# Optimization experiments

Hardware: AMD Instinct MI355X
Metric: run time of the kernel (lower is better)

The kernel has to match this reference:

```python
import jax, jax.numpy as jnp
import numpy as np

KERNEL_SIZE = 32
KERNEL_STRIDE = 16
HEAD_NUM_K = 4
HEAD_DIM = 128
BATCH = 4
SEQ_LEN = 16384


def _calc_chunks_with_stride(cu_seqlens_np, chunk_size, stride):
    """Mirror of calc_chunks_with_stride using numpy (index computation on host).

    Returns flat gather indices (num_chunks*chunk_size,) and compressed
    cumulative sequence lengths (batch+1,).
    """
    cu = np.asarray(cu_seqlens_np, dtype=np.int64)
    batch_sizes = cu[1:] - cu[:-1]
    max_seq_len = int(batch_sizes.max())
    max_chunks = max((max_seq_len - chunk_size) // stride + 1, 0)
    offsets = np.arange(0, max_chunks * stride, stride, dtype=np.int64)  # (C,)
    seq_starts = cu[:-1]
    chunk_start = seq_starts[:, None] + offsets[None, :]            # (B, C)
    chunk_end = chunk_start + chunk_size
    valid = chunk_end <= (seq_starts[:, None] + batch_sizes[:, None])  # (B, C)
    valid_starts = chunk_start[valid]                               # (N,)
    inner = np.arange(chunk_size, dtype=np.int64)[None, :]          # (1, K)
    flat_idx = (valid_starts[:, None] + inner).reshape(-1)          # (N*K,)
    n_per_batch = valid.sum(axis=1)
    cu_comp = np.zeros(len(cu), dtype=np.int32)
    cu_comp[1:] = np.cumsum(n_per_batch)
    return flat_idx, cu_comp


def setup_inputs() -> dict:
    key = jax.random.key(0)
    k = jax.random.normal(key, (BATCH * SEQ_LEN, HEAD_NUM_K, HEAD_DIM), dtype=jnp.float32)
    cu_seqlens = jnp.arange(BATCH + 1, dtype=jnp.int32) * SEQ_LEN
    return {"k": k, "cu_seqlens": cu_seqlens}


def reference(k, cu_seqlens):
    # Index computation is data-dependent on concrete cu_seqlens (host-side).
    flat_idx, cu_comp = _calc_chunks_with_stride(np.asarray(cu_seqlens), KERNEL_SIZE, KERNEL_STRIDE)
    idx = jnp.asarray(flat_idx)
    # Gather overlapping chunks: (N*K, H, D) -> (N, K, H, D) -> mean over K.
    gathered = k[idx]
    gathered = gathered.reshape(-1, KERNEL_SIZE, HEAD_NUM_K, HEAD_DIM)
    compressed_k = gathered.mean(axis=1)
    return compressed_k, jnp.asarray(cu_comp)
```

## Files before the change

kernel.cpp:

```cpp
#include <hip/hip_runtime.h>

#define KSIZE   32
#define KSTRIDE 16
#define HK      4
#define HD      128
#define ROW     (HK * HD)
#define ROW4    (ROW / 4)
#define BATCH   4
#define SEQLEN  16384
#define CHUNKS_PER_BATCH ((SEQLEN - KSIZE) / KSTRIDE + 1)
#define TOTAL_CHUNKS     (BATCH * CHUNKS_PER_BATCH)
#define HW_PER_BATCH     (SEQLEN / KSTRIDE)
#define TOTAL_HW         (BATCH * HW_PER_BATCH)
#define WS_FLOATS        ((size_t)TOTAL_HW * ROW)


__global__ __launch_bounds__(128)
void hw_sums(const float* __restrict__ k,
             const int* __restrict__ cu_seqlens,
             float* __restrict__ H) {
    const int j  = blockIdx.x;
    const int b  = j >> 10;
    const int hw = j & (HW_PER_BATCH - 1);
    const float4* __restrict__ src = (const float4*)
        (k + ((long)cu_seqlens[b] + (long)hw * KSTRIDE) * ROW);
    const int t = threadIdx.x;

    float4 a0 = make_float4(0.f, 0.f, 0.f, 0.f);
    float4 a1 = make_float4(0.f, 0.f, 0.f, 0.f);
    #pragma unroll
    for (int r = 0; r < KSTRIDE; r += 2) {
        float4 u = src[(long)r * ROW4 + t];
        float4 v = src[(long)(r + 1) * ROW4 + t];
        a0.x += u.x; a0.y += u.y; a0.z += u.z; a0.w += u.w;
        a1.x += v.x; a1.y += v.y; a1.z += v.z; a1.w += v.w;
    }
    float4 s = make_float4(a0.x + a1.x, a0.y + a1.y, a0.z + a1.z, a0.w + a1.w);
    ((float4*)(H + (long)j * ROW))[t] = s;
}

__global__ __launch_bounds__(256)
void hw_combine(const float* __restrict__ H,
                const int* __restrict__ cu_seqlens,
                float* __restrict__ out,
                float* __restrict__ tail) {
    const int idx = blockIdx.x * 256 + threadIdx.x;
    if (idx < TOTAL_CHUNKS * ROW4) {
        const int chunk = idx >> 7;
        const int col   = idx & (ROW4 - 1);
        const int b     = chunk / CHUNKS_PER_BATCH;
        const int c     = chunk - b * CHUNKS_PER_BATCH;

        const long h = ((long)(b * HW_PER_BATCH + c)) * ROW4 + col;
        float4 u = ((const float4*)H)[h];
        float4 v = ((const float4*)H)[h + ROW4];
        const float s = 1.0f / (float)KSIZE;
        float4 r = make_float4((u.x + v.x) * s, (u.y + v.y) * s,
                               (u.z + v.z) * s, (u.w + v.w) * s);
        ((float4*)out)[(long)chunk * ROW4 + col] = r;
    }

    if (idx == 0) {
        int run = 0;
        tail[0] = 0.0f;
        #pragma unroll
        for (int i = 0; i < BATCH; ++i) {
            const int len = cu_seqlens[i + 1] - cu_seqlens[i];
            const int n = (len >= KSIZE) ? (len - KSIZE) / KSTRIDE + 1 : 0;
            run += n;
            tail[i + 1] = (float)run;
        }
    }
}

#define SPAN 8
#define FB_BLOCKS_PER_BATCH ((CHUNKS_PER_BATCH + SPAN - 1) / SPAN)
#define FB_TOTAL_BLOCKS     (BATCH * FB_BLOCKS_PER_BATCH)

__device__ __forceinline__ float4 sum16(const float4* __restrict__ src,
                                        int row0, int t) {
    float4 a0 = make_float4(0.f, 0.f, 0.f, 0.f);
    float4 a1 = make_float4(0.f, 0.f, 0.f, 0.f);
    #pragma unroll
    for (int i = 0; i < 8; ++i) {
        float4 u = src[(long)(row0 + 2 * i)     * ROW4 + t];
        float4 v = src[(long)(row0 + 2 * i + 1) * ROW4 + t];
        a0.x += u.x; a0.y += u.y; a0.z += u.z; a0.w += u.w;
        a1.x += v.x; a1.y += v.y; a1.z += v.z; a1.w += v.w;
    }
    a0.x += a1.x; a0.y += a1.y; a0.z += a1.z; a0.w += a1.w;
    return a0;
}

__global__ __launch_bounds__(128)
void compress_k_fallback(const float* __restrict__ k,
                         const int* __restrict__ cu_seqlens,
                         float* __restrict__ out,
                         float* __restrict__ tail) {
    const int blk = blockIdx.x;
    const int b   = blk / FB_BLOCKS_PER_BATCH;
    const int cb  = blk - b * FB_BLOCKS_PER_BATCH;
    const int c0  = cb * SPAN;
    const int gc  = (CHUNKS_PER_BATCH - c0 < SPAN) ? (CHUNKS_PER_BATCH - c0)
                                                   : SPAN;
    const float4* __restrict__ src = (const float4*)
        (k + ((long)cu_seqlens[b] + (long)c0 * KSTRIDE) * ROW);
    const int t = threadIdx.x;
    const float s = 1.0f / (float)KSIZE;
    float* outp = out + (long)(b * CHUNKS_PER_BATCH + c0) * ROW;

    float4 prev = sum16(src, 0, t);
    for (int g = 0; g < gc; ++g) {
        float4 cur = sum16(src, (g + 1) * KSTRIDE, t);
        float4 r = make_float4((prev.x + cur.x) * s, (prev.y + cur.y) * s,
                               (prev.z + cur.z) * s, (prev.w + cur.w) * s);
        ((float4*)(outp + (long)g * ROW))[t] = r;
        prev = cur;
    }
    if (blk == 0 && t == 0) {
        int run = 0;
        tail[0] = 0.0f;
        #pragma unroll
        for (int i = 0; i < BATCH; ++i) {
            const int len = cu_seqlens[i + 1] - cu_seqlens[i];
            const int n = (len >= KSIZE) ? (len - KSIZE) / KSTRIDE + 1 : 0;
            run += n;
            tail[i + 1] = (float)run;
        }
    }
}

extern "C" void kernel_launch(void* const* d_in, const int* in_sizes, int n_in,
                              void* d_out, int out_size, void* d_ws, size_t ws_size,
                              hipStream_t stream) {
    const float* k          = (const float*)d_in[0];
    const int*   cu_seqlens = (const int*)d_in[1];
    float*       out        = (float*)d_out;
    float*       tail       = out + (long)TOTAL_CHUNKS * ROW;

    if (ws_size >= WS_FLOATS * sizeof(float) && d_ws != nullptr) {
        float* H = (float*)d_ws;
        hw_sums<<<TOTAL_HW, 128, 0, stream>>>(k, cu_seqlens, H);
        const int p2_threads = TOTAL_CHUNKS * ROW4;
        const int p2_blocks  = (p2_threads + 255) / 256;
        hw_combine<<<p2_blocks, 256, 0, stream>>>(H, cu_seqlens, out, tail);
    } else {
        compress_k_fallback<<<FB_TOTAL_BLOCKS, 128, 0, stream>>>(
            k, cu_seqlens, out, tail);
    }
}
```

Before: 195.6 us.

## Compute even chunks inside the partial-sum pass and combine only odd chunks after

The first pass now handles two consecutive stride-16 windows per block, writes both partial sums to the workspace, and directly emits the even-indexed compressed chunk. The second pass only combines partial sums for odd-indexed chunks, halving its reads and writes. This trades fewer, larger first-pass blocks for less intermediate memory traffic in the second kernel.

```diff
diff --git a/kernel.cpp b/kernel.cpp
--- a/kernel.cpp
+++ b/kernel.cpp
@@ -15,52 +15,54 @@
 #define WS_FLOATS        ((size_t)TOTAL_HW * ROW)
 
 
+#define P1_BLOCKS_PER_BATCH (HW_PER_BATCH / 2)
+#define P1_TOTAL_BLOCKS     (BATCH * P1_BLOCKS_PER_BATCH)
+#define ODD_PER_BATCH       (CHUNKS_PER_BATCH / 2)
+#define TOTAL_ODD           (BATCH * ODD_PER_BATCH)
+#define P2_THREADS          (TOTAL_ODD * ROW4)
+#define P2_BLOCKS           (P2_THREADS / 256)
+
 __global__ __launch_bounds__(128)
-void hw_sums(const float* __restrict__ k,
+void hw_even(const float* __restrict__ k,
              const int* __restrict__ cu_seqlens,
-             float* __restrict__ H) {
-    const int j  = blockIdx.x;
-    const int b  = j >> 10;
-    const int hw = j & (HW_PER_BATCH - 1);
+             float* __restrict__ H,
+             float* __restrict__ out,
+             float* __restrict__ tail) {
+    const int blk = blockIdx.x;
+    const int b   = blk >> 9;
+    const int m   = blk & (P1_BLOCKS_PER_BATCH - 1);
     const float4* __restrict__ src = (const float4*)
-        (k + ((long)cu_seqlens[b] + (long)hw * KSTRIDE) * ROW);
+        (k + ((long)cu_seqlens[b] + (long)m * KSIZE) * ROW);
     const int t = threadIdx.x;
 
     float4 a0 = make_float4(0.f, 0.f, 0.f, 0.f);
     float4 a1 = make_float4(0.f, 0.f, 0.f, 0.f);
+    float4 a2 = make_float4(0.f, 0.f, 0.f, 0.f);
+    float4 a3 = make_float4(0.f, 0.f, 0.f, 0.f);
     #pragma unroll
-    for (int r = 0; r < KSTRIDE; r += 2) {
-        float4 u = src[(long)r * ROW4 + t];
-        float4 v = src[(long)(r + 1) * ROW4 + t];
-        a0.x += u.x; a0.y += u.y; a0.z += u.z; a0.w += u.w;
-        a1.x += v.x; a1.y += v.y; a1.z += v.z; a1.w += v.w;
+    for (int i = 0; i < 8; ++i) {
+        float4 u0 = src[(long)(2 * i)               * ROW4 + t];
+        float4 v0 = src[(long)(2 * i + 1)           * ROW4 + t];
+        float4 u1 = src[(long)(KSTRIDE + 2 * i)     * ROW4 + t];
+        float4 v1 = src[(long)(KSTRIDE + 2 * i + 1) * ROW4 + t];
+        a0.x += u0.x; a0.y += u0.y; a0.z += u0.z; a0.w += u0.w;
+        a1.x += v0.x; a1.y += v0.y; a1.z += v0.z; a1.w += v0.w;
+        a2.x += u1.x; a2.y += u1.y; a2.z += u1.z; a2.w += u1.w;
+        a3.x += v1.x; a3.y += v1.y; a3.z += v1.z; a3.w += v1.w;
     }
-    float4 s = make_float4(a0.x + a1.x, a0.y + a1.y, a0.z + a1.z, a0.w + a1.w);
-    ((float4*)(H + (long)j * ROW))[t] = s;
-}
+    float4 h0 = make_float4(a0.x + a1.x, a0.y + a1.y, a0.z + a1.z, a0.w + a1.w);
+    float4 h1 = make_float4(a2.x + a3.x, a2.y + a3.y, a2.z + a3.z, a2.w + a3.w);
 
-__global__ __launch_bounds__(256)
-void hw_combine(const float* __restrict__ H,
-                const int* __restrict__ cu_seqlens,
-                float* __restrict__ out,
-                float* __restrict__ tail) {
-    const int idx = blockIdx.x * 256 + threadIdx.x;
-    if (idx < TOTAL_CHUNKS * ROW4) {
-        const int chunk = idx >> 7;
-        const int col   = idx & (ROW4 - 1);
-        const int b     = chunk / CHUNKS_PER_BATCH;
-        const int c     = chunk - b * CHUNKS_PER_BATCH;
+    float4* Hp = (float4*)H + ((long)(b * HW_PER_BATCH + 2 * m)) * ROW4 + t;
+    Hp[0]    = h0;
+    Hp[ROW4] = h1;
 
-        const long h = ((long)(b * HW_PER_BATCH + c)) * ROW4 + col;
-        float4 u = ((const float4*)H)[h];
-        float4 v = ((const float4*)H)[h + ROW4];
-        const float s = 1.0f / (float)KSIZE;
-        float4 r = make_float4((u.x + v.x) * s, (u.y + v.y) * s,
-                               (u.z + v.z) * s, (u.w + v.w) * s);
-        ((float4*)out)[(long)chunk * ROW4 + col] = r;
-    }
+    const float s = 1.0f / (float)KSIZE;
+    float4 r = make_float4((h0.x + h1.x) * s, (h0.y + h1.y) * s,
+                           (h0.z + h1.z) * s, (h0.w + h1.w) * s);
+    ((float4*)out)[((long)(b * CHUNKS_PER_BATCH + 2 * m)) * ROW4 + t] = r;
 
-    if (idx == 0) {
+    if (blk == 0 && t == 0) {
         int run = 0;
         tail[0] = 0.0f;
         #pragma unroll
@@ -71,6 +73,25 @@
             tail[i + 1] = (float)run;
         }
     }
+}
+
+__global__ __launch_bounds__(256)
+void hw_odd(const float* __restrict__ H,
+            float* __restrict__ out) {
+    const int idx = blockIdx.x * 256 + threadIdx.x;
+    const int q   = idx >> 7;
+    const int col = idx & (ROW4 - 1);
+    const int b   = q / ODD_PER_BATCH;
+    const int j   = q - b * ODD_PER_BATCH;
+    const int c   = 2 * j + 1;
+
+    const long h = ((long)(b * HW_PER_BATCH + c)) * ROW4 + col;
+    float4 u = ((const float4*)H)[h];
+    float4 v = ((const float4*)H)[h + ROW4];
+    const float s = 1.0f / (float)KSIZE;
+    float4 r = make_float4((u.x + v.x) * s, (u.y + v.y) * s,
+                           (u.z + v.z) * s, (u.w + v.w) * s);
+    ((float4*)out)[((long)(b * CHUNKS_PER_BATCH + c)) * ROW4 + col] = r;
 }
 
 #define SPAN 8
@@ -140,10 +161,8 @@
 
     if (ws_size >= WS_FLOATS * sizeof(float) && d_ws != nullptr) {
         float* H = (float*)d_ws;
-        hw_sums<<<TOTAL_HW, 128, 0, stream>>>(k, cu_seqlens, H);
-        const int p2_threads = TOTAL_CHUNKS * ROW4;
-        const int p2_blocks  = (p2_threads + 255) / 256;
-        hw_combine<<<p2_blocks, 256, 0, stream>>>(H, cu_seqlens, out, tail);
+        hw_even<<<P1_TOTAL_BLOCKS, 128, 0, stream>>>(k, cu_seqlens, H, out, tail);
+        hw_odd<<<P2_BLOCKS, 256, 0, stream>>>(H, out);
     } else {
         compress_k_fallback<<<FB_TOTAL_BLOCKS, 128, 0, stream>>>(
             k, cu_seqlens, out, tail);
```

New measurement: 198.3 us. Within noise of the previous version (+1.4%).
